# Performance work log

Measured on AMD Instinct MI355X. Metric: run time of the kernel, lower is better.

Reference implementation:

```python
import jax, jax.numpy as jnp
import numpy as np


def setup_inputs() -> dict:
    key = jax.random.key(0)
    ks = jax.random.split(key, 8)
    B, L, D, H = 4, 2048, 4096, 8
    BW = D // H
    std = 1.0 / np.sqrt(BW)
    x = jax.random.normal(ks[0], (B, L, D), dtype=jnp.float32)
    segment_pos = jax.random.randint(ks[1], (B, L), 0, 1024)
    prev_h = jax.random.normal(ks[2], (B, D), dtype=jnp.float32)
    w_in = jax.random.normal(ks[3], (H, BW, BW), dtype=jnp.float32) * std
    b_in = jnp.zeros((H, BW), dtype=jnp.float32)
    w_a = jax.random.normal(ks[4], (H, BW, BW), dtype=jnp.float32) * std
    b_a = jnp.zeros((H, BW), dtype=jnp.float32)
    # a_param init: uniform on ring [0.9, 0.999], softplus-inverse transform
    unif = jax.random.uniform(ks[5], (D,), dtype=jnp.float32)
    min_rad, max_rad = 0.9, 0.999
    a_real = 0.5 * jnp.log(unif * (max_rad**2 - min_rad**2) + min_rad**2 + 1e-8)
    a_param = jnp.log(jnp.exp(-a_real) - 1.0)
    return {"x": x, "segment_pos": segment_pos, "prev_h": prev_h,
            "w_in": w_in, "b_in": b_in, "w_a": w_a, "b_a": b_a,
            "a_param": a_param}


def _block_diag_linear(x, w, b):
    # x: [B,L,D]; w: [H,BW,BW]; b: [H,BW]
    B, L, D = x.shape
    H = w.shape[0]
    xr = x.reshape(B, L, H, D // H)
    y = jnp.einsum('blhi,hij->blhj', xr, w) + b
    return y.reshape(B, L, D)


def reference(x, segment_pos, prev_h, w_in, b_in, w_a, b_a, a_param):
    # reset indicator at document boundaries (segment_pos == 0)
    reset = (segment_pos == 0).astype(x.dtype)          # [B,L]
    gate_x = jax.nn.sigmoid(_block_diag_linear(x, w_in, b_in))
    gate_a = jax.nn.sigmoid(_block_diag_linear(x, w_a, b_a))
    log_a = -8.0 * gate_a * jax.nn.softplus(a_param)    # [B,L,D]
    a = jnp.exp(log_a)
    multiplier = jnp.sqrt(1.0 - jnp.exp(2.0 * log_a) + 1e-6)
    multiplier = reset[..., None] + (1.0 - reset)[..., None] * multiplier
    normalized_x = x * gate_x * multiplier
    # zero the decay at reset positions (hidden state reset)
    a = a * (1.0 - reset)[..., None]
    # linear recurrence y_t = a_t * y_{t-1} + x_t (initial hidden state = 0,
    # matching the torch L>1 path which does not use prev_h)
    def combine(c1, c2):
        a1, b1 = c1
        a2, b2 = c2
        return (a2 * a1, a2 * b1 + b2)
    _, y = jax.lax.associative_scan(combine, (a, normalized_x), axis=1)
    return y
```

## Files before the change

kernel.cpp:

```cpp
#include <hip/hip_runtime.h>
#include <hip/hip_bf16.h>

typedef _Float16 f16;
typedef _Float16 f16x2 __attribute__((ext_vector_type(2)));
typedef _Float16 f16x4 __attribute__((ext_vector_type(4)));
typedef _Float16 f16x8 __attribute__((ext_vector_type(8)));
typedef float f32x4 __attribute__((ext_vector_type(4)));

#define B_  4
#define L_  2048
#define D_  4096
#define H_  8
#define BW_ 512
#define M_  (B_*L_)
#define CHUNK 128
#define NCH (L_/CHUNK)
#define LOG2E 1.4426950408889634f

static const size_t OFF_WTIN  = 0;
static const size_t OFF_WTA   = 4ull<<20;
static const size_t OFF_MSP   = 8ull<<20;
static const size_t OFF_XH    = 9ull<<20;
static const size_t OFF_YLAP  = 73ull<<20;
static const size_t OFF_SUMA  = 208ull<<20;
static const size_t OFF_SUMY  = 209ull<<20;
static const size_t OFF_CARRY = 210ull<<20;

__device__ __forceinline__ void gl16(const void* g, void* l) {
    __builtin_amdgcn_global_load_lds(
        (const __attribute__((address_space(1))) unsigned int*)g,
        (__attribute__((address_space(3))) unsigned int*)l, 16, 0, 0);
}

__global__ __launch_bounds__(256)
void prep_weights(const float* __restrict__ w_in, const float* __restrict__ w_a,
                  f16* __restrict__ wtin, f16* __restrict__ wta) {
    __shared__ float tile[32][33];
    int g = blockIdx.z >> 3;
    int h = blockIdx.z & 7;
    const float* src = (g ? w_a : w_in) + (size_t)h * BW_ * BW_;
    f16* dst = (g ? wta : wtin) + (size_t)h * BW_ * BW_;
    int i0 = blockIdx.y * 32, j0 = blockIdx.x * 32;
    int tx = threadIdx.x & 31, ty = threadIdx.x >> 5;
#pragma unroll
    for (int q = 0; q < 4; ++q) {
        int i = ty + q * 8;
        tile[i][tx] = src[(size_t)(i0 + i) * BW_ + j0 + tx];
    }
    __syncthreads();
#pragma unroll
    for (int q = 0; q < 4; ++q) {
        int j = ty + q * 8;
        dst[(size_t)(j0 + j) * BW_ + i0 + tx] = (f16)tile[tx][j];
    }
}

__global__ __launch_bounds__(256)
void prep_msp(const float* __restrict__ a_param, float* __restrict__ msp2) {
    int d = blockIdx.x * 256 + threadIdx.x;
    float v = a_param[d];
    msp2[d] = -8.f * log1pf(expf(v)) * LOG2E;
}

__global__ __launch_bounds__(256)
void prep_xh(const float* __restrict__ x, f16* __restrict__ xh) {
    size_t i = ((size_t)blockIdx.x * 256 + threadIdx.x) * 8;
    size_t stride = (size_t)gridDim.x * 256 * 8;
    for (; i < (size_t)M_ * D_; i += stride) {
        f32x4 v0 = *(const f32x4*)(x + i);
        f32x4 v1 = *(const f32x4*)(x + i + 4);
        f16x8 hv;
        hv[0] = (f16)v0.x; hv[1] = (f16)v0.y; hv[2] = (f16)v0.z; hv[3] = (f16)v0.w;
        hv[4] = (f16)v1.x; hv[5] = (f16)v1.y; hv[6] = (f16)v1.z; hv[7] = (f16)v1.w;
        *(f16x8*)(xh + i) = hv;
    }
}

#define BM 128
#define BN 64
#define BKK 64
#define NT (BW_/BKK)
#define BUFB 32768
#define SMEM_BYTES 65536

__global__ __launch_bounds__(256)
void gemm_gates(const f16*   __restrict__ xh,
                const int*   __restrict__ segpos,
                const f16*   __restrict__ wtin,
                const f16*   __restrict__ wta,
                const float* __restrict__ b_in,
                const float* __restrict__ b_a,
                const float* __restrict__ msp2,
                f16x2* __restrict__ ylap,
                float* __restrict__ sumA,
                float* __restrict__ sumY) {
    __shared__ __align__(16) char smem[SMEM_BYTES];
    float* a_s  = (float*)smem;
    f16*   xn_s = (f16*)(smem + 33280);
    float* segA = (float*)(smem + 50176);
    float* segY = (float*)(smem + 51328);

    const int tid  = threadIdx.x;
    const int m0   = blockIdx.x * BM;
    const int n0   = blockIdx.y * BN;
    const int h    = blockIdx.z;
    const int lane = tid & 63;
    const int wid  = tid >> 6;
    const int wr   = wid >> 1;
    const int wc   = wid & 1;

    f32x4 accX[4][2] = {};
    f32x4 accA[4][2] = {};

    const int grow  = lane >> 3;
    const int gcolS = (((lane & 7) ^ grow) << 3);
    const f16* aSrc  = xh   + (size_t)(m0 + wid * 32 + grow) * D_ + h * BW_ + gcolS;
    const f16* bxSrc = wtin + ((size_t)h * BW_ + n0 + wid * 16 + grow) * BW_ + gcolS;
    const f16* baSrc = wta  + ((size_t)h * BW_ + n0 + wid * 16 + grow) * BW_ + gcolS;

    const int swz  = (lane & 7) << 3;
    const int kx   = (lane >> 4) << 3;
    const int arow = wr * 64 + (lane & 15);
    const int brow = wc * 32 + (lane & 15);

    const int rowb = wr * 64 + ((lane >> 4) << 2);
    int rmask = 0;
#pragma unroll
    for (int fm = 0; fm < 4; ++fm)
#pragma unroll
        for (int reg = 0; reg < 4; ++reg)
            if (segpos[m0 + rowb + fm * 16 + reg] == 0) rmask |= 1 << (fm * 4 + reg);

    const int txo = (n0 >> 6) + 1;

    {
        const int k0 = ((txo) & (NT - 1)) * BKK;
        char* base = smem;
        f16* Asb = (f16*)base;
        f16* Bxb = (f16*)(base + 16384);
        f16* Bab = (f16*)(base + 24576);
#pragma unroll
        for (int q = 0; q < 4; ++q)
            gl16(aSrc + k0 + (size_t)q * 8 * D_, &Asb[(wid * 32 + q * 8) * 64]);
#pragma unroll
        for (int q = 0; q < 2; ++q) {
            gl16(bxSrc + k0 + (size_t)q * 8 * BW_, &Bxb[(wid * 16 + q * 8) * 64]);
            gl16(baSrc + k0 + (size_t)q * 8 * BW_, &Bab[(wid * 16 + q * 8) * 64]);
        }
    }

#pragma unroll
    for (int t = 0; t < NT; ++t) {
        const int cur = t & 1;
        if (t + 1 < NT) {
            const int k1 = ((t + 1 + txo) & (NT - 1)) * BKK;
            char* base = smem + (cur ^ 1) * BUFB;
            f16* Asb = (f16*)base;
            f16* Bxb = (f16*)(base + 16384);
            f16* Bab = (f16*)(base + 24576);
#pragma unroll
            for (int q = 0; q < 4; ++q)
                gl16(aSrc + k1 + (size_t)q * 8 * D_, &Asb[(wid * 32 + q * 8) * 64]);
#pragma unroll
            for (int q = 0; q < 2; ++q) {
                gl16(bxSrc + k1 + (size_t)q * 8 * BW_, &Bxb[(wid * 16 + q * 8) * 64]);
                gl16(baSrc + k1 + (size_t)q * 8 * BW_, &Bab[(wid * 16 + q * 8) * 64]);
            }
            asm volatile("s_waitcnt vmcnt(8)" ::: "memory");
        } else {
            asm volatile("s_waitcnt vmcnt(0)" ::: "memory");
        }
        __builtin_amdgcn_s_barrier();
        __builtin_amdgcn_sched_barrier(0);

        const f16* Asb = (const f16*)(smem + cur * BUFB);
        const f16* Bxb = (const f16*)(smem + cur * BUFB + 16384);
        const f16* Bab = (const f16*)(smem + cur * BUFB + 24576);
#pragma unroll
        for (int kk = 0; kk < BKK; kk += 32) {
            const int kcolS = (kk + kx) ^ swz;
            f16x8 af[4];
#pragma unroll
            for (int fm = 0; fm < 4; ++fm)
                af[fm] = *(const f16x8*)&Asb[(arow + fm * 16) * 64 + kcolS];
#pragma unroll
            for (int fn = 0; fn < 2; ++fn) {
                f16x8 bx = *(const f16x8*)&Bxb[(brow + fn * 16) * 64 + kcolS];
                f16x8 ba = *(const f16x8*)&Bab[(brow + fn * 16) * 64 + kcolS];
#pragma unroll
                for (int fm = 0; fm < 4; ++fm) {
                    accX[fm][fn] = __builtin_amdgcn_mfma_f32_16x16x32_f16(af[fm], bx, accX[fm][fn], 0, 0, 0);
                    accA[fm][fn] = __builtin_amdgcn_mfma_f32_16x16x32_f16(af[fm], ba, accA[fm][fn], 0, 0, 0);
                }
            }
        }
        __builtin_amdgcn_sched_barrier(0);
        __builtin_amdgcn_s_barrier();
    }

    const f16* As1 = (const f16*)(smem + ((NT - 1) & 1) * BUFB);
    f16 xvv[2][4][4];
#pragma unroll
    for (int fn = 0; fn < 2; ++fn) {
        const int ctile = wc * 32 + fn * 16 + (lane & 15);
#pragma unroll
        for (int fm = 0; fm < 4; ++fm)
#pragma unroll
            for (int reg = 0; reg < 4; ++reg) {
                const int rowt = rowb + fm * 16 + reg;
                xvv[fn][fm][reg] = As1[rowt * 64 + (ctile ^ ((rowt & 7) << 3))];
            }
    }
    __syncthreads();

    {
#pragma unroll
        for (int fn = 0; fn < 2; ++fn) {
            const int ctile = wc * 32 + fn * 16 + (lane & 15);
            const int d = h * BW_ + n0 + ctile;
            const float bx = b_in[d];
            const float ba = b_a[d];
            const float mspd = msp2[d];
#pragma unroll
            for (int fm = 0; fm < 4; ++fm) {
#pragma unroll
                for (int reg = 0; reg < 4; ++reg) {
                    const int rowt = rowb + fm * 16 + reg;
                    float gxl = accX[fm][fn][reg] + bx;
                    float gal = accA[fm][fn][reg] + ba;
                    float gx = __builtin_amdgcn_rcpf(1.f + __builtin_amdgcn_exp2f(-gxl * LOG2E));
                    float ga = __builtin_amdgcn_rcpf(1.f + __builtin_amdgcn_exp2f(-gal * LOG2E));
                    float a  = __builtin_amdgcn_exp2f(mspd * ga);
                    float a2 = a * a;
                    float mult = __builtin_amdgcn_sqrtf(1.f + 1e-6f - a2);
                    float rv = ((rmask >> (fm * 4 + reg)) & 1) ? 1.f : 0.f;
                    a *= (1.f - rv);
                    mult = rv + (1.f - rv) * mult;
                    float xv = (float)xvv[fn][fm][reg];
                    a_s[rowt * 65 + ctile] = a;
                    xn_s[rowt * 66 + ctile] = (f16)(xv * gx * mult);
                }
            }
        }
    }
    __syncthreads();

    const int scol = tid & 63;
    const int sseg = tid >> 6;
    {
        float A = 1.f, yv = 0.f;
#pragma unroll 4
        for (int t = sseg * 32; t < sseg * 32 + 32; ++t) {
            float a  = a_s[t * 65 + scol];
            float xn = (float)xn_s[t * 66 + scol];
            yv = fmaf(a, yv, xn);
            A *= a;
        }
        segA[sseg * 72 + scol] = A;
        segY[sseg * 72 + scol] = yv;
    }
    __syncthreads();

    {
        float cy = 0.f, pA = 1.f;
        for (int s = 0; s < sseg; ++s) {
            float As_ = segA[s * 72 + scol];
            float Ys_ = segY[s * 72 + scol];
            cy = fmaf(As_, cy, Ys_);
            pA *= As_;
        }
        float Arun = 1.f, yv = cy;
        const size_t obase = (size_t)(m0 + sseg * 32) * D_ + h * BW_ + n0 + scol;
#pragma unroll 4
        for (int i = 0; i < 32; ++i) {
            const int t = sseg * 32 + i;
            float a  = a_s[t * 65 + scol];
            float xn = (float)xn_s[t * 66 + scol];
            yv = fmaf(a, yv, xn);
            Arun *= a;
            f16x2 p;
            p[0] = (f16)yv;
            p[1] = (f16)(pA * Arun);
            ylap[obase + (size_t)i * D_] = p;
        }
        if (sseg == 3) {
            const int bb = m0 >> 11;
            const int cc = (m0 & 2047) >> 7;
            size_t si = ((size_t)bb * NCH + cc) * D_ + h * BW_ + n0 + scol;
            sumA[si] = pA * Arun;
            sumY[si] = yv;
        }
    }
}

__global__ __launch_bounds__(256)
void scan_mid(const float* __restrict__ sumA, const float* __restrict__ sumY,
              float* __restrict__ carry) {
    int d = blockIdx.x * 256 + threadIdx.x;
    int b = blockIdx.y;
    float hcur = 0.f;
#pragma unroll
    for (int c = 0; c < NCH; ++c) {
        size_t si = ((size_t)b * NCH + c) * D_ + d;
        carry[si] = hcur;
        hcur = fmaf(sumA[si], hcur, sumY[si]);
    }
}

__global__ __launch_bounds__(256)
void scan_apply(const float* __restrict__ carry, const f16x2* __restrict__ ylap,
                float* __restrict__ y) {
    size_t i4 = (size_t)blockIdx.x * 256 + threadIdx.x;
    const size_t stride = (size_t)gridDim.x * 256;
    const size_t n4 = (size_t)M_ * D_ / 4;
    for (; i4 < n4; i4 += stride) {
        size_t i = i4 * 4;
        size_t row = i >> 12;
        int d = (int)(i & 4095);
        int b = (int)(row >> 11);
        int c = ((int)row & 2047) >> 7;
        const float* cp = carry + (((size_t)(b * NCH + c)) << 12) + d;
        f32x4 cv = *(const f32x4*)cp;
        f16x8 pk = *(const f16x8*)(ylap + i);
        f32x4 o;
        o.x = fmaf(cv.x, (float)pk[1], (float)pk[0]);
        o.y = fmaf(cv.y, (float)pk[3], (float)pk[2]);
        o.z = fmaf(cv.z, (float)pk[5], (float)pk[4]);
        o.w = fmaf(cv.w, (float)pk[7], (float)pk[6]);
        *(f32x4*)(y + i) = o;
    }
}

extern "C" void kernel_launch(void* const* d_in, const int* in_sizes, int n_in,
                              void* d_out, int out_size, void* d_ws, size_t ws_size,
                              hipStream_t stream) {
    const float* x       = (const float*)d_in[0];
    const int*   segpos  = (const int*)d_in[1];
    const float* w_in    = (const float*)d_in[3];
    const float* b_in    = (const float*)d_in[4];
    const float* w_a     = (const float*)d_in[5];
    const float* b_a     = (const float*)d_in[6];
    const float* a_param = (const float*)d_in[7];

    float* y  = (float*)d_out;
    char*  ws = (char*)d_ws;
    f16*   wtin  = (f16*)(ws + OFF_WTIN);
    f16*   wta   = (f16*)(ws + OFF_WTA);
    float* msp2  = (float*)(ws + OFF_MSP);
    f16*   xh    = (f16*)(ws + OFF_XH);
    f16x2* ylap  = (f16x2*)(ws + OFF_YLAP);
    float* sumA  = (float*)(ws + OFF_SUMA);
    float* sumY  = (float*)(ws + OFF_SUMY);
    float* carry = (float*)(ws + OFF_CARRY);

    prep_weights<<<dim3(16, 16, 16), 256, 0, stream>>>(w_in, w_a, wtin, wta);
    prep_msp<<<dim3(D_ / 256), 256, 0, stream>>>(a_param, msp2);
    prep_xh<<<dim3(2048), 256, 0, stream>>>(x, xh);
    gemm_gates<<<dim3(M_ / BM, BW_ / BN, H_), 256, 0, stream>>>(
        xh, segpos, wtin, wta, b_in, b_a, msp2, ylap, sumA, sumY);
    scan_mid<<<dim3(D_ / 256, B_), 256, 0, stream>>>(sumA, sumY, carry);
    scan_apply<<<dim3(4096), 256, 0, stream>>>(carry, ylap, y);
}
```

Baseline: 239.0 us.

## Prepack weights into MFMA fragment order and load B directly to registers

Weights are repacked in a prep kernel into per-lane MFMA fragment layout so the GEMM loads B operands straight from global memory into registers, double-buffered, instead of staging them through LDS. This halves the LDS buffer size, lowering shared memory so occupancy can rise to three blocks per CU, with launch bounds set to match. Reset flags now come from a small LDS array instead of per-thread global segpos reads and a bitmask. The trade-off is more VGPR pressure from holding two sets of B fragments, and redundant global B reads across waves that LDS used to share.

```diff
diff --git a/kernel.cpp b/kernel.cpp
--- a/kernel.cpp
+++ b/kernel.cpp
@@ -17,8 +17,7 @@
 #define NCH (L_/CHUNK)
 #define LOG2E 1.4426950408889634f
 
-static const size_t OFF_WTIN  = 0;
-static const size_t OFF_WTA   = 4ull<<20;
+static const size_t OFF_WPK   = 0;
 static const size_t OFF_MSP   = 8ull<<20;
 static const size_t OFF_XH    = 9ull<<20;
 static const size_t OFF_YLAP  = 73ull<<20;
@@ -33,25 +32,29 @@
 }
 
 __global__ __launch_bounds__(256)
-void prep_weights(const float* __restrict__ w_in, const float* __restrict__ w_a,
-                  f16* __restrict__ wtin, f16* __restrict__ wta) {
-    __shared__ float tile[32][33];
-    int g = blockIdx.z >> 3;
-    int h = blockIdx.z & 7;
-    const float* src = (g ? w_a : w_in) + (size_t)h * BW_ * BW_;
-    f16* dst = (g ? wta : wtin) + (size_t)h * BW_ * BW_;
-    int i0 = blockIdx.y * 32, j0 = blockIdx.x * 32;
-    int tx = threadIdx.x & 31, ty = threadIdx.x >> 5;
-#pragma unroll
-    for (int q = 0; q < 4; ++q) {
-        int i = ty + q * 8;
-        tile[i][tx] = src[(size_t)(i0 + i) * BW_ + j0 + tx];
-    }
-    __syncthreads();
-#pragma unroll
-    for (int q = 0; q < 4; ++q) {
-        int j = ty + q * 8;
-        dst[(size_t)(j0 + j) * BW_ + i0 + tx] = (f16)tile[tx][j];
+void prep_wpack(const float* __restrict__ w_in, const float* __restrict__ w_a,
+                f16* __restrict__ wpk) {
+    const int kt  = blockIdx.x & 7;
+    const int n32 = (blockIdx.x >> 3) & 15;
+    const int h   = blockIdx.x >> 7;
+    const int tid = threadIdx.x;
+#pragma unroll
+    for (int q = 0; q < 2; ++q) {
+        int slot = q * 256 + tid;
+        int lane = slot & 63;
+        int fidx = slot >> 6;
+        int g    = fidx >> 2;
+        int fn   = (fidx >> 1) & 1;
+        int kk2  = fidx & 1;
+        int row = n32 * 32 + fn * 16 + (lane & 15);
+        int col = kt * 64 + kk2 * 32 + ((lane >> 4) << 3);
+        const float* src = (g ? w_a : w_in) + (size_t)h * BW_ * BW_;
+        f16x8 v;
+#pragma unroll
+        for (int e = 0; e < 8; ++e)
+            v[e] = (f16)src[(size_t)(col + e) * BW_ + row];
+        size_t o = ((((size_t)(h * 16 + n32) * 8 + kt) * 8) + fidx) * 64 + lane;
+        *(f16x8*)(wpk + o * 8) = v;
     }
 }
 
@@ -80,14 +83,14 @@
 #define BN 64
 #define BKK 64
 #define NT (BW_/BKK)
-#define BUFB 32768
-#define SMEM_BYTES 65536
-
-__global__ __launch_bounds__(256)
+#define BUFB 16384
+
+#define SMEM_BYTES 52992
+
+__global__ __launch_bounds__(256, 3)
 void gemm_gates(const f16*   __restrict__ xh,
                 const int*   __restrict__ segpos,
-                const f16*   __restrict__ wtin,
-                const f16*   __restrict__ wta,
+                const f16*   __restrict__ wpk,
                 const float* __restrict__ b_in,
                 const float* __restrict__ b_a,
                 const float* __restrict__ msp2,
@@ -99,6 +102,7 @@
     f16*   xn_s = (f16*)(smem + 33280);
     float* segA = (float*)(smem + 50176);
     float* segY = (float*)(smem + 51328);
+    float* rst_s= (float*)(smem + 52480);
 
     const int tid  = threadIdx.x;
     const int m0   = blockIdx.x * BM;
@@ -112,61 +116,49 @@
     f32x4 accX[4][2] = {};
     f32x4 accA[4][2] = {};
 
+    if (tid < BM) rst_s[tid] = (segpos[m0 + tid] == 0) ? 1.f : 0.f;
+
     const int grow  = lane >> 3;
     const int gcolS = (((lane & 7) ^ grow) << 3);
-    const f16* aSrc  = xh   + (size_t)(m0 + wid * 32 + grow) * D_ + h * BW_ + gcolS;
-    const f16* bxSrc = wtin + ((size_t)h * BW_ + n0 + wid * 16 + grow) * BW_ + gcolS;
-    const f16* baSrc = wta  + ((size_t)h * BW_ + n0 + wid * 16 + grow) * BW_ + gcolS;
+    const f16* aSrc = xh + (size_t)(m0 + wid * 32 + grow) * D_ + h * BW_ + gcolS;
+
+    const f16* wbase = wpk + ((size_t)(h * 16) + (n0 >> 5) + wc) * 32768;
 
     const int swz  = (lane & 7) << 3;
     const int kx   = (lane >> 4) << 3;
     const int arow = wr * 64 + (lane & 15);
-    const int brow = wc * 32 + (lane & 15);
 
     const int rowb = wr * 64 + ((lane >> 4) << 2);
-    int rmask = 0;
-#pragma unroll
-    for (int fm = 0; fm < 4; ++fm)
-#pragma unroll
-        for (int reg = 0; reg < 4; ++reg)
-            if (segpos[m0 + rowb + fm * 16 + reg] == 0) rmask |= 1 << (fm * 4 + reg);
-
     const int txo = (n0 >> 6) + 1;
 
+    f16x8 bfr[2][8];
+
     {
-        const int k0 = ((txo) & (NT - 1)) * BKK;
-        char* base = smem;
-        f16* Asb = (f16*)base;
-        f16* Bxb = (f16*)(base + 16384);
-        f16* Bab = (f16*)(base + 24576);
+        const int k0 = (txo & (NT - 1)) * BKK;
+        f16* Asb = (f16*)smem;
 #pragma unroll
         for (int q = 0; q < 4; ++q)
             gl16(aSrc + k0 + (size_t)q * 8 * D_, &Asb[(wid * 32 + q * 8) * 64]);
-#pragma unroll
-        for (int q = 0; q < 2; ++q) {
-            gl16(bxSrc + k0 + (size_t)q * 8 * BW_, &Bxb[(wid * 16 + q * 8) * 64]);
-            gl16(baSrc + k0 + (size_t)q * 8 * BW_, &Bab[(wid * 16 + q * 8) * 64]);
-        }
+        const f16* tp = wbase + (size_t)(txo & (NT - 1)) * 4096;
+#pragma unroll
+        for (int j = 0; j < 8; ++j)
+            bfr[0][j] = *(const f16x8*)(tp + j * 512 + lane * 8);
     }
 
 #pragma unroll
     for (int t = 0; t < NT; ++t) {
         const int cur = t & 1;
         if (t + 1 < NT) {
-            const int k1 = ((t + 1 + txo) & (NT - 1)) * BKK;
-            char* base = smem + (cur ^ 1) * BUFB;
-            f16* Asb = (f16*)base;
-            f16* Bxb = (f16*)(base + 16384);
-            f16* Bab = (f16*)(base + 24576);
+            const int kt1 = (t + 1 + txo) & (NT - 1);
+            f16* Asb = (f16*)(smem + (cur ^ 1) * BUFB);
 #pragma unroll
             for (int q = 0; q < 4; ++q)
-                gl16(aSrc + k1 + (size_t)q * 8 * D_, &Asb[(wid * 32 + q * 8) * 64]);
-#pragma unroll
-            for (int q = 0; q < 2; ++q) {
-                gl16(bxSrc + k1 + (size_t)q * 8 * BW_, &Bxb[(wid * 16 + q * 8) * 64]);
-                gl16(baSrc + k1 + (size_t)q * 8 * BW_, &Bab[(wid * 16 + q * 8) * 64]);
-            }
-            asm volatile("s_waitcnt vmcnt(8)" ::: "memory");
+                gl16(aSrc + kt1 * BKK + (size_t)q * 8 * D_, &Asb[(wid * 32 + q * 8) * 64]);
+            const f16* tp = wbase + (size_t)kt1 * 4096;
+#pragma unroll
+            for (int j = 0; j < 8; ++j)
+                bfr[cur ^ 1][j] = *(const f16x8*)(tp + j * 512 + lane * 8);
+            asm volatile("s_waitcnt vmcnt(12)" ::: "memory");
         } else {
             asm volatile("s_waitcnt vmcnt(0)" ::: "memory");
         }
@@ -174,19 +166,17 @@
         __builtin_amdgcn_sched_barrier(0);
 
         const f16* Asb = (const f16*)(smem + cur * BUFB);
-        const f16* Bxb = (const f16*)(smem + cur * BUFB + 16384);
-        const f16* Bab = (const f16*)(smem + cur * BUFB + 24576);
-#pragma unroll
-        for (int kk = 0; kk < BKK; kk += 32) {
-            const int kcolS = (kk + kx) ^ swz;
+#pragma unroll
+        for (int kk2 = 0; kk2 < 2; ++kk2) {
+            const int kcolS = (kk2 * 32 + kx) ^ swz;
             f16x8 af[4];
 #pragma unroll
             for (int fm = 0; fm < 4; ++fm)
                 af[fm] = *(const f16x8*)&Asb[(arow + fm * 16) * 64 + kcolS];
 #pragma unroll
             for (int fn = 0; fn < 2; ++fn) {
-                f16x8 bx = *(const f16x8*)&Bxb[(brow + fn * 16) * 64 + kcolS];
-                f16x8 ba = *(const f16x8*)&Bab[(brow + fn * 16) * 64 + kcolS];
+                f16x8 bx = bfr[cur][fn * 2 + kk2];
+                f16x8 ba = bfr[cur][4 + fn * 2 + kk2];
 #pragma unroll
                 for (int fm = 0; fm < 4; ++fm) {
                     accX[fm][fn] = __builtin_amdgcn_mfma_f32_16x16x32_f16(af[fm], bx, accX[fm][fn], 0, 0, 0);
@@ -198,7 +188,7 @@
         __builtin_amdgcn_s_barrier();
     }
 
-    const f16* As1 = (const f16*)(smem + ((NT - 1) & 1) * BUFB);
+    const f16* As1 = (const f16*)(smem + BUFB);
     f16 xvv[2][4][4];
 #pragma unroll
     for (int fn = 0; fn < 2; ++fn) {
@@ -233,7 +223,7 @@
                     float a  = __builtin_amdgcn_exp2f(mspd * ga);
                     float a2 = a * a;
                     float mult = __builtin_amdgcn_sqrtf(1.f + 1e-6f - a2);
-                    float rv = ((rmask >> (fm * 4 + reg)) & 1) ? 1.f : 0.f;
+                    float rv = rst_s[rowt];
                     a *= (1.f - rv);
                     mult = rv + (1.f - rv) * mult;
                     float xv = (float)xvv[fn][fm][reg];
@@ -344,8 +334,7 @@
 
     float* y  = (float*)d_out;
     char*  ws = (char*)d_ws;
-    f16*   wtin  = (f16*)(ws + OFF_WTIN);
-    f16*   wta   = (f16*)(ws + OFF_WTA);
+    f16*   wpk   = (f16*)(ws + OFF_WPK);
     float* msp2  = (float*)(ws + OFF_MSP);
     f16*   xh    = (f16*)(ws + OFF_XH);
     f16x2* ylap  = (f16x2*)(ws + OFF_YLAP);
@@ -353,11 +342,11 @@
     float* sumY  = (float*)(ws + OFF_SUMY);
     float* carry = (float*)(ws + OFF_CARRY);
 
-    prep_weights<<<dim3(16, 16, 16), 256, 0, stream>>>(w_in, w_a, wtin, wta);
+    prep_wpack<<<dim3(1024), 256, 0, stream>>>(w_in, w_a, wpk);
     prep_msp<<<dim3(D_ / 256), 256, 0, stream>>>(a_param, msp2);
     prep_xh<<<dim3(2048), 256, 0, stream>>>(x, xh);
     gemm_gates<<<dim3(M_ / BM, BW_ / BN, H_), 256, 0, stream>>>(
-        xh, segpos, wtin, wta, b_in, b_a, msp2, ylap, sumA, sumY);
+        xh, segpos, wpk, b_in, b_a, msp2, ylap, sumA, sumY);
     scan_mid<<<dim3(D_ / 256, B_), 256, 0, stream>>>(sumA, sumY, carry);
     scan_apply<<<dim3(4096), 256, 0, stream>>>(carry, ylap, y);
 }
```

New measurement: 223.5 us. 1.07x faster.
